# Kernel optimization log

Measured on AMD Instinct MI355X. Metric: run time of the kernel, lower is better.

## Reference

```python
import jax, jax.numpy as jnp
import numpy as np

B, N, DEG = 8, 8192, 16
E = B * N * DEG
K1 = 2458  # ceil(0.3*8192)
K2 = 738   # ceil(0.3*2458)
NUM_CLASSES = 10


def gat(x, src, dst, emask, W, a_s, a_d, bias):
    # PyG GATConv with add_self_loops=True, negative_slope=0.2, concat heads
    n = x.shape[0]
    H, F = a_s.shape
    xp = (x @ W).reshape(n, H, F)                      # [n,H,F]
    al_s = (xp * a_s).sum(-1)                          # [n,H]
    al_d = (xp * a_d).sum(-1)
    loops = jnp.arange(n, dtype=src.dtype)
    s2 = jnp.concatenate([src, loops])
    d2 = jnp.concatenate([dst, loops])
    m2 = jnp.concatenate([emask, jnp.ones(n, bool)])
    e = jax.nn.leaky_relu(al_s[s2] + al_d[d2], 0.2)    # [E+n,H]
    e = jnp.where(m2[:, None], e, -1e9)
    emax = jax.ops.segment_max(e, d2, num_segments=n)
    ex = jnp.where(m2[:, None], jnp.exp(e - emax[d2]), 0.0)
    den = jax.ops.segment_sum(ex, d2, num_segments=n)
    msg = ex[:, :, None] * xp[s2]                      # [E+n,H,F]
    out = jax.ops.segment_sum(msg, d2, num_segments=n) / den[:, :, None]
    return out.reshape(n, H * F) + bias


def inorm(x):
    # PyG InstanceNorm (affine=False): per-graph per-channel normalization
    xb = x.reshape(B, -1, x.shape[-1])
    mu = xb.mean(1, keepdims=True)
    var = ((xb - mu) ** 2).mean(1, keepdims=True)
    return ((xb - mu) / jnp.sqrt(var + 1e-5)).reshape(x.shape)


def topk_pool(x, src, dst, emask, p, k):
    # TopKPooling: score = tanh(x.p/|p|), keep top-k per graph, scale x by score
    n_tot = x.shape[0]
    n = n_tot // B
    score = jnp.tanh((x @ p) / jnp.linalg.norm(p))
    sv, si = jax.lax.top_k(score.reshape(B, n), k)     # [B,k]
    xg = jnp.take_along_axis(x.reshape(B, n, -1), si[:, :, None], axis=1)
    xnew = (xg * sv[:, :, None]).reshape(B * k, -1)
    perm = (si + (jnp.arange(B) * n)[:, None]).reshape(-1)
    newid = jnp.full(n_tot, -1, dtype=src.dtype).at[perm].set(
        jnp.arange(B * k, dtype=src.dtype))
    ns, nd = newid[src], newid[dst]
    m = emask & (ns >= 0) & (nd >= 0)
    return xnew, jnp.maximum(ns, 0), jnp.maximum(nd, 0), m


def setup_inputs() -> dict:
    key = jax.random.key(0)
    ks = jax.random.split(key, 32)
    pos = jax.random.normal(ks[0], (B * N, 3), jnp.float32)
    offs = jnp.repeat(jnp.arange(B, dtype=jnp.int32) * N, N * DEG)
    src = jax.random.randint(ks[1], (E,), 0, N, jnp.int32) + offs
    dst = jax.random.randint(ks[2], (E,), 0, N, jnp.int32) + offs

    def lin(k, fi, fo):
        return jax.random.normal(k, (fi, fo), jnp.float32) * (1.0 / np.sqrt(fi))

    d = dict(pos=pos, src=src, dst=dst)
    d['W1'] = lin(ks[3], 3, 32);   d['a_s1'] = jax.random.normal(ks[4], (2, 16)) * 0.2
    d['a_d1'] = jax.random.normal(ks[5], (2, 16)) * 0.2
    d['b1'] = jnp.zeros((32,));    d['p1'] = jax.random.normal(ks[6], (32,))
    d['W2'] = lin(ks[7], 32, 128); d['a_s2'] = jax.random.normal(ks[8], (2, 64)) * 0.2
    d['a_d2'] = jax.random.normal(ks[9], (2, 64)) * 0.2
    d['b2'] = jnp.zeros((128,));   d['p2'] = jax.random.normal(ks[10], (128,))
    d['W3'] = lin(ks[11], 128, 256); d['a_s3'] = jax.random.normal(ks[12], (1, 256)) * 0.1
    d['a_d3'] = jax.random.normal(ks[13], (1, 256)) * 0.1
    d['b3'] = jnp.zeros((256,))
    d['gw1'] = lin(ks[14], 256, 64);  d['gb1'] = jnp.zeros((64,))
    d['gw2'] = lin(ks[15], 64, 1);    d['gb2'] = jnp.zeros((1,))
    d['aw'] = lin(ks[16], 256, 256);  d['ab'] = jnp.zeros((256,))
    d['w1'] = lin(ks[17], 256, 512);  d['bb1'] = jnp.zeros((512,))
    d['w2'] = lin(ks[18], 512, 128);  d['bb2'] = jnp.zeros((128,))
    d['w3'] = lin(ks[19], 128, NUM_CLASSES); d['bb3'] = jnp.zeros((NUM_CLASSES,))
    return d


def reference(pos, src, dst, W1, a_s1, a_d1, b1, p1, W2, a_s2, a_d2, b2, p2,
              W3, a_s3, a_d3, b3, gw1, gb1, gw2, gb2, aw, ab,
              w1, bb1, w2, bb2, w3, bb3):
    emask = jnp.ones(src.shape[0], bool)
    x = gat(pos, src, dst, emask, W1, a_s1, a_d1, b1)
    x = jax.nn.elu(inorm(x))
    x, src, dst, emask = topk_pool(x, src, dst, emask, p1, K1)
    x = gat(x, src, dst, emask, W2, a_s2, a_d2, b2)
    x = jax.nn.elu(inorm(x))
    x, src, dst, emask = topk_pool(x, src, dst, emask, p2, K2)
    x = gat(x, src, dst, emask, W3, a_s3, a_d3, b3)
    x = jax.nn.elu(inorm(x))
    # GlobalAttention: gate_nn = Linear(256,64)+ELU+Linear(64,1); nn = Linear+ELU
    gate = jax.nn.elu(x @ gw1 + gb1) @ gw2 + gb2       # [M,1]
    h = jax.nn.elu(x @ aw + ab)                        # [M,256]
    a = jax.nn.softmax(gate.reshape(B, K2, 1), axis=1)
    g = (a * h.reshape(B, K2, 256)).sum(1)             # [B,256]
    z = jax.nn.elu(g @ w1 + bb1)   # dropout inactive in eval
    z = jax.nn.elu(z @ w2 + bb2)
    z = z @ w3 + bb3
    return jax.nn.log_softmax(z, axis=1)
```

## Files before the change

kernel.cpp:

```cpp
#include <hip/hip_runtime.h>
#include <cstdint>
#include <cstddef>

#define DI __device__ __forceinline__

namespace pk {

constexpr int NB1 = 65536;
constexpr int NE  = 1048576;
constexpr int BG  = 8;
constexpr int NPG1 = 8192;
constexpr int EPG1 = NE/BG;
constexpr int KP1 = 2458;
constexpr int KP2 = 738;
constexpr int NN2 = BG*KP1;
constexpr int NN3 = BG*KP2;
constexpr int REG2 = 16384;
constexpr int REG3 = 4096;
constexpr int CAP2 = BG*REG2;
constexpr int CAP3 = BG*REG3;
constexpr int CPB1 = 8;
constexpr int NTILE = 32;
constexpr int BKT = 5120;

DI float lrelu(float x){ return x > 0.f ? x : 0.2f*x; }
DI float eluf(float x){ return x > 0.f ? x : expf(x) - 1.f; }

DI int swz_block(){
  int nb = gridDim.x, b = blockIdx.x;
  if((nb & 7) == 0) return (b & 7)*(nb >> 3) + (b >> 3);
  return b;
}

__global__ __launch_bounds__(1024) void k_s1_front(
    const float* __restrict__ pos, const float* __restrict__ W,
    const float* __restrict__ as_, const float* __restrict__ ad_,
    float* __restrict__ xp, float* __restrict__ als, float* __restrict__ ald,
    const int* __restrict__ se, const int* __restrict__ de,
    int* __restrict__ part, int* __restrict__ bcur, int* __restrict__ bpk){
  __shared__ int h[NPG1];
  __shared__ int hbase[NTILE];
  __shared__ int hc[NTILE];
  int tid = threadIdx.x;
  if(blockIdx.x < 64){
    int i = blockIdx.x*1024 + tid;
    float p0=pos[3*i], p1=pos[3*i+1], p2=pos[3*i+2];
    float row[32];
#pragma unroll
    for(int c=0;c<32;c++) row[c] = p0*W[c] + p1*W[32+c] + p2*W[64+c];
    float s0=0.f,d0=0.f,s1=0.f,d1=0.f;
#pragma unroll
    for(int f=0;f<16;f++){
      s0 += row[f]*as_[f];        d0 += row[f]*ad_[f];
      s1 += row[16+f]*as_[16+f];  d1 += row[16+f]*ad_[16+f];
    }
    float4* o = reinterpret_cast<float4*>(xp + (size_t)i*32);
#pragma unroll
    for(int q=0;q<8;q++) o[q] = make_float4(row[4*q],row[4*q+1],row[4*q+2],row[4*q+3]);
    als[2*i]=s0; als[2*i+1]=s1; ald[2*i]=d0; ald[2*i+1]=d1;
    return;
  }
  int bb = blockIdx.x - 64;
  int g = bb & 7, t = bb >> 3;
  for(int i=tid;i<NPG1;i+=1024) h[i]=0;
  __syncthreads();
  const int4* de4 = (const int4*)(de + g*EPG1 + t*(EPG1/CPB1));
  const int4* se4 = (const int4*)(se + g*EPG1 + t*(EPG1/CPB1));
  int lo = g*NPG1;
  int4 dv[4], sv[4];
#pragma unroll
  for(int j=0;j<4;j++){ dv[j]=de4[j*1024+tid]; sv[j]=se4[j*1024+tid]; }
  int dl[16], sl[16];
#pragma unroll
  for(int j=0;j<4;j++){
    dl[4*j+0]=dv[j].x-lo; dl[4*j+1]=dv[j].y-lo; dl[4*j+2]=dv[j].z-lo; dl[4*j+3]=dv[j].w-lo;
    sl[4*j+0]=sv[j].x-lo; sl[4*j+1]=sv[j].y-lo; sl[4*j+2]=sv[j].z-lo; sl[4*j+3]=sv[j].w-lo;
  }
#pragma unroll
  for(int q=0;q<16;q++) atomicAdd(&h[dl[q]],1);
  __syncthreads();
  if(tid < NTILE){
    int ssum = 0;
    for(int i=0;i<256;i++) ssum += h[tid*256+i];
    hbase[tid] = atomicAdd(&bcur[g*NTILE+tid], ssum);
    hc[tid] = 0;
  }
  int* pp = part + (size_t)(g*CPB1+t)*NPG1;
  for(int i=tid;i<NPG1;i+=1024) pp[i]=h[i];
  __syncthreads();
#pragma unroll
  for(int q=0;q<16;q++){
    int tt = dl[q] >> 8;
    int p = atomicAdd(&hc[tt],1) + hbase[tt];
    bpk[(size_t)(g*NTILE+tt)*BKT + p] = (sl[q]<<13) | dl[q];
  }
}

__global__ __launch_bounds__(1024) void k_scan1(
    const int* __restrict__ part, int* __restrict__ cnt,
    int* __restrict__ rowptr){
  __shared__ int wsum[16];
  int g = blockIdx.x;
  int tid = threadIdx.x, lane = tid & 63, w = tid >> 6;
  constexpr int PER = NPG1/1024;
  int base = g*NPG1;
  int i0 = tid*PER;
  int v[PER]; int s = 0;
#pragma unroll
  for(int j=0;j<PER;j++){
    int i = i0+j;
    int x = 0;
#pragma unroll
    for(int p=0;p<CPB1;p++) x += part[(size_t)(g*CPB1+p)*NPG1 + i];
    cnt[base+i] = x;
    v[j] = s; s += x;
  }
  int inc = s;
  for(int o=1;o<64;o<<=1){ int t2=__shfl_up(inc,o,64); if(lane>=o) inc+=t2; }
  if(lane==63) wsum[w]=inc;
  __syncthreads();
  int wb=0;
  for(int k=0;k<w;k++) wb+=wsum[k];
  int tb = g*EPG1 + wb + inc - s;
#pragma unroll
  for(int j=0;j<PER;j++) rowptr[base+i0+j] = tb + v[j];
}

__global__ __launch_bounds__(1024) void k_scatter_b(
    const int* __restrict__ bcur, const int* __restrict__ bpk,
    const int* __restrict__ rowptr, int* __restrict__ eo){
  __shared__ int cur[256];
  int tid = threadIdx.x;
  int g = blockIdx.x & 7, t = blockIdx.x >> 3;
  int lo = g*NPG1 + t*256;
  if(tid < 256) cur[tid] = rowptr[lo + tid];
  __syncthreads();
  int cnt = bcur[g*NTILE + t];
  const int* bp = bpk + (size_t)(g*NTILE + t)*BKT;
  for(int i=tid; i<cnt; i+=1024){
    int pk = bp[i];
    int dlo = pk & 8191;
    int slo = pk >> 13;
    int p = atomicAdd(&cur[dlo - t*256], 1);
    eo[p] = g*NPG1 + slo;
  }
}

__global__ __launch_bounds__(256) void k_scatter_r(
    const int* __restrict__ se, const int* __restrict__ de,
    const int* __restrict__ gcnt, int reg,
    int* __restrict__ cursor, int* __restrict__ eo){
  int i = swz_block()*256 + threadIdx.x;
  int g = i / reg, loc = i % reg;
  if(loc < gcnt[g]){
    int p = atomicAdd(&cursor[de[i]], 1);
    eo[p] = se[i];
  }
}

__global__ __launch_bounds__(256) void k_edge_compact(
    const int* __restrict__ se, const int* __restrict__ de,
    const int* __restrict__ gcnt_in, int fixed_in, int bpg, int reg_in,
    const int* __restrict__ newid, int* __restrict__ gcnt_out,
    int* __restrict__ ons, int* __restrict__ ond, int reg_out,
    int* __restrict__ cnt){
  __shared__ int s_a[4096];
  __shared__ int s_b[4096];
  __shared__ int run, tbase;
  int tid = threadIdx.x;
  if(tid == 0) run = 0;
  __syncthreads();
  int blk = swz_block();
  int g = blk / bpg, t = blk % bpg;
  int mg = gcnt_in ? gcnt_in[g] : fixed_in;
  if(mg > reg_in) mg = reg_in;
  int base_l = t*4096;
  if(base_l < mg){
    const int* deb = de + (size_t)g*reg_in + base_l;
    const int* seb = se + (size_t)g*reg_in + base_l;
    const int4* de4 = (const int4*)deb;
    const int4* se4 = (const int4*)seb;
    int4 BD[4], BS[4];
#pragma unroll
    for(int j=0;j<4;j++){ BD[j]=de4[j*256+tid]; BS[j]=se4[j*256+tid]; }
    int cl = 0;
#pragma unroll
    for(int j=0;j<4;j++){
      int eb = base_l + (j*256+tid)*4;
      int dd[4]={BD[j].x,BD[j].y,BD[j].z,BD[j].w};
      int ss[4]={BS[j].x,BS[j].y,BS[j].z,BS[j].w};
#pragma unroll
      for(int q=0;q<4;q++){
        if(eb+q < mg){
          int a = newid[ss[q]], b = newid[dd[q]];
          if(a>=0 && b>=0){ cl++; atomicAdd(&cnt[b], 1); }
        }
      }
    }
    int p0 = 0;
    if(cl) p0 = atomicAdd(&run, cl);
#pragma unroll
    for(int j=0;j<4;j++){
      int eb = base_l + (j*256+tid)*4;
      int dd[4]={BD[j].x,BD[j].y,BD[j].z,BD[j].w};
      int ss[4]={BS[j].x,BS[j].y,BS[j].z,BS[j].w};
#pragma unroll
      for(int q=0;q<4;q++){
        if(eb+q < mg){
          int a = newid[ss[q]], b = newid[dd[q]];
          if(a>=0 && b>=0){ s_a[p0]=a; s_b[p0]=b; p0++; }
        }
      }
    }
  }
  __syncthreads();
  int ns = run;
  if(tid==0) tbase = ns ? atomicAdd(&gcnt_out[g], ns) : 0;
  __syncthreads();
  int tb = tbase;
  for(int j=tid; j<ns; j+=256){
    int s2 = tb + j;
    if(s2 < reg_out){ ons[(size_t)g*reg_out+s2]=s_a[j]; ond[(size_t)g*reg_out+s2]=s_b[j]; }
  }
}

template<int PER>
DI void scan256(const int* __restrict__ cnt, int R, int estride,
                int* __restrict__ rowptr, int* __restrict__ cursor, int g){
  __shared__ int wsum[4];
  int tid = threadIdx.x, lane = tid & 63, w = tid >> 6;
  int base = g*R;
  int i0 = tid*PER;
  int v[PER]; int s = 0;
#pragma unroll
  for(int j=0;j<PER;j++){ int i=i0+j; int x=(i<R)?cnt[base+i]:0; v[j]=s; s+=x; }
  int inc = s;
  for(int o=1;o<64;o<<=1){ int t=__shfl_up(inc,o,64); if(lane>=o) inc+=t; }
  if(lane==63) wsum[w]=inc;
  __syncthreads();
  int wb=0;
  for(int k=0;k<w;k++) wb+=wsum[k];
  int tb = g*estride + wb + inc - s;
#pragma unroll
  for(int j=0;j<PER;j++){
    int i=i0+j;
    if(i<R){
      int e=tb+v[j];
      rowptr[base+i]=e;
      cursor[base+i]=e;
    }
  }
}

template<int H,int F,int EB>
__global__ __launch_bounds__(256) void k_gat_fused(
    const float* __restrict__ xp, const float* __restrict__ als,
    const float* __restrict__ ald, const int* __restrict__ rowptr,
    const int* __restrict__ cnt, const int* __restrict__ esrc,
    const float* __restrict__ bias, float* __restrict__ out,
    float* __restrict__ accum, int RPG, int bpg){
  constexpr int C = H*F, C4 = C/4;
  constexpr int NPB = 256/C4;
  __shared__ float psum[4][C], psq[4][C];
  int tid = threadIdx.x;
  int nl = tid / C4, p = tid % C4;
  int work = (blockIdx.x & 7)*(gridDim.x >> 3) + (blockIdx.x >> 3);
  int g = work / bpg, t = work - g*bpg;
  int loc = t*NPB + nl;
  int node = g*RPG + loc;
  int hh = (4*p)/F;
  const float4* xp4 = (const float4*)xp;
  float4 r = make_float4(0.f,0.f,0.f,0.f);
  bool valid = loc < RPG;
  if(valid){
    float dvh = ald[node*H+hh];
    float sw  = expf(lrelu(als[node*H+hh] + dvh));
    float4 xs = xp4[(size_t)node*C4 + p];
    float den = sw;
    float ax=sw*xs.x, ay=sw*xs.y, az=sw*xs.z, aw_=sw*xs.w;
    int r0  = rowptr[node];
    int deg = cnt[node];
    for(int j=0; j<deg; j+=EB){
      int idx[EB]; float wv[EB]; float4 v[EB];
#pragma unroll
      for(int q=0;q<EB;q++)
        idx[q] = (j+q < deg) ? esrc[r0+j+q] : node;
#pragma unroll
      for(int q=0;q<EB;q++)
        wv[q] = als[idx[q]*H+hh];
#pragma unroll
      for(int q=0;q<EB;q++)
        v[q] = xp4[(size_t)idx[q]*C4 + p];
#pragma unroll
      for(int q=0;q<EB;q++){
        float w = (j+q < deg) ? expf(lrelu(wv[q] + dvh)) : 0.f;
        den += w;
        ax += w*v[q].x; ay += w*v[q].y; az += w*v[q].z; aw_ += w*v[q].w;
      }
    }
    float inv = 1.f / den;
    float4 bv = ((const float4*)bias)[p];
    r.x=ax*inv+bv.x; r.y=ay*inv+bv.y; r.z=az*inv+bv.z; r.w=aw_*inv+bv.w;
    ((float4*)out)[(size_t)node*C4 + p] = r;
  }
  float sx=r.x, sy=r.y, sz=r.z, sw2=r.w;
  float qx=r.x*r.x, qy=r.y*r.y, qz=r.z*r.z, qw=r.w*r.w;
#pragma unroll
  for(int off=C4; off<64; off<<=1){
    sx += __shfl_down(sx, off, 64); sy += __shfl_down(sy, off, 64);
    sz += __shfl_down(sz, off, 64); sw2 += __shfl_down(sw2, off, 64);
    qx += __shfl_down(qx, off, 64); qy += __shfl_down(qy, off, 64);
    qz += __shfl_down(qz, off, 64); qw += __shfl_down(qw, off, 64);
  }
  int lane = tid & 63, w = tid >> 6;
  if(lane < C4){
    psum[w][4*lane+0]=sx; psum[w][4*lane+1]=sy;
    psum[w][4*lane+2]=sz; psum[w][4*lane+3]=sw2;
    psq[w][4*lane+0]=qx;  psq[w][4*lane+1]=qy;
    psq[w][4*lane+2]=qz;  psq[w][4*lane+3]=qw;
  }
  __syncthreads();
  if(tid < C){
    float ts = psum[0][tid]+psum[1][tid]+psum[2][tid]+psum[3][tid];
    float tq = psq[0][tid]+psq[1][tid]+psq[2][tid]+psq[3][tid];
    atomicAdd(&accum[(g*C+tid)*2],   ts);
    atomicAdd(&accum[(g*C+tid)*2+1], tq);
  }
}

DI float inorm_of(const float* accum, int gc, float R, float x){
  float s = accum[gc*2], sq = accum[gc*2+1];
  float mu = s / R;
  float var = fmaxf(sq/R - mu*mu, 0.f);
  return eluf((x-mu)*rsqrtf(var+1e-5f));
}

template<int K,int CO,int NPG,int H,int PER>
__global__ __launch_bounds__(256) void k_gemm_al(
    const float* __restrict__ X, const float* __restrict__ naccum, int nRPG,
    const int* __restrict__ oldid,
    const float* __restrict__ scale, const float* __restrict__ W,
    float* __restrict__ Y, const float* __restrict__ a_s,
    const float* __restrict__ a_d, float* __restrict__ als,
    float* __restrict__ ald, int n, int ngemm,
    const int* __restrict__ scnt, int sR, int sstride,
    int* __restrict__ srowptr, int* __restrict__ scursor){
  constexpr int SUB = 256/CO;
  constexpr int NB = SUB*NPG;
  __shared__ float xs[NB][K];
  __shared__ float ps[4][NPG], pd[4][NPG];
  if((int)blockIdx.x >= ngemm){
    scan256<PER>(scnt, sR, sstride, srowptr, scursor, (int)blockIdx.x - ngemm);
    return;
  }
  int tid = threadIdx.x;
  int c = tid % CO, sg = tid / CO;
  int n0 = blockIdx.x * NB;
  for(int idx=tid; idx<NB*K; idx+=256){
    int r = idx / K, k = idx % K;
    int row = n0 + r;
    float v = 0.f;
    if(row < n){
      int orow = oldid[row];
      int og = orow / nRPG;
      v = inorm_of(naccum, og*K + k, (float)nRPG, X[(size_t)orow*K + k]) * scale[row];
    }
    xs[r][k] = v;
  }
  __syncthreads();
  float acc[NPG];
#pragma unroll
  for(int q=0;q<NPG;q++) acc[q]=0.f;
  for(int k=0;k<K;k++){
    float wv = W[(size_t)k*CO + c];
#pragma unroll
    for(int q=0;q<NPG;q++) acc[q] += xs[sg*NPG+q][k]*wv;
  }
  float asc = a_s[c], adc = a_d[c];
  float vs[NPG], vd[NPG];
#pragma unroll
  for(int q=0;q<NPG;q++){
    int row = n0 + sg*NPG + q;
    if(row < n) Y[(size_t)row*CO + c] = acc[q];
    vs[q] = acc[q]*asc; vd[q] = acc[q]*adc;
  }
#pragma unroll
  for(int o=32;o>0;o>>=1){
#pragma unroll
    for(int q=0;q<NPG;q++){
      vs[q] += __shfl_down(vs[q], o, 64);
      vd[q] += __shfl_down(vd[q], o, 64);
    }
  }
  int lane = tid & 63, w = tid >> 6;
  if(H == 2){
    if(lane == 0){
      int sg_ = w >> 1, h = w & 1;
#pragma unroll
      for(int q=0;q<NPG;q++){
        int row = n0 + sg_*NPG + q;
        if(row < n){ als[row*2+h] = vs[q]; ald[row*2+h] = vd[q]; }
      }
    }
  } else {
    if(lane == 0){
#pragma unroll
      for(int q=0;q<NPG;q++){ ps[w][q]=vs[q]; pd[w][q]=vd[q]; }
    }
    __syncthreads();
    if(tid < NPG){
      float s=0.f, d=0.f;
      for(int ww=0;ww<4;ww++){ s+=ps[ww][tid]; d+=pd[ww][tid]; }
      int row = n0 + tid;
      if(row < n){ als[row]=s; ald[row]=d; }
    }
  }
}

template<int C>
__global__ __launch_bounds__(256) void k_inorm_score(
    const float* __restrict__ x, const float* __restrict__ accum,
    const float* __restrict__ p, int R, int total,
    float* __restrict__ score, unsigned* __restrict__ u){
  __shared__ float rvp[256], rpp[256];
  int tid = threadIdx.x;
  int i = blockIdx.x*256 + tid;
  int c = tid & (C-1);
  bool act = i < total;
  float v = 0.f, pv = 0.f;
  if(act){
    int g = i / (R*C);
    v = inorm_of(accum, g*C+c, (float)R, x[i]);
    pv = p[c];
  }
  rvp[tid] = v*pv; rpp[tid] = pv*pv;
  __syncthreads();
#pragma unroll
  for(int s2=C/2; s2>0; s2>>=1){
    if(c < s2){ rvp[tid]+=rvp[tid+s2]; rpp[tid]+=rpp[tid+s2]; }
    __syncthreads();
  }
  if(act && c==0){
    float sv = tanhf(rvp[tid]*rsqrtf(rpp[tid]));
    int row = i / C;
    score[row] = sv;
    unsigned bts = __float_as_uint(sv);
    u[row] = (bts & 0x80000000u) ? ~bts : (bts | 0x80000000u);
  }
}

__global__ __launch_bounds__(1024) void k_topk(
    const unsigned* __restrict__ u, const float* __restrict__ score,
    int R, int Ksel, int* __restrict__ newid, int* __restrict__ oldid,
    float* __restrict__ scale){
  __shared__ int hist[2048];
  __shared__ int seg[32];
  __shared__ int sh_b, sh_k;
  __shared__ int wsA[16], wsB[16];
  __shared__ int carr0, carr1;
  int g = blockIdx.x, tid = threadIdx.x, lane = tid&63, w = tid>>6;
  const unsigned* ug = u + (size_t)g*R;
  unsigned prefix = 0;
  int K = Ksel;
  for(int lev=0; lev<3; lev++){
    int shf = (lev==0)?21:((lev==1)?10:0);
    int nb  = (lev==2)?1024:2048;
    for(int i=tid;i<2048;i+=1024) hist[i]=0;
    __syncthreads();
    for(int i=tid;i<R;i+=1024){
      unsigned v = ug[i];
      bool ok = (lev==0) || (lev==1 && (v>>21)==prefix) || (lev==2 && (v>>10)==prefix);
      if(ok) atomicAdd(&hist[(v>>shf)&(nb-1)], 1);
    }
    __syncthreads();
    int W = nb/32;
    if(tid<32){ int s=0; int lo=nb-W*(tid+1); for(int b=lo;b<lo+W;b++) s+=hist[b]; seg[tid]=s; }
    __syncthreads();
    if(tid==0){
      int kk=K, sgi=0;
      while(seg[sgi]<kk){ kk-=seg[sgi]; sgi++; }
      int b = nb-1-W*sgi;
      while(hist[b]<kk){ kk-=hist[b]; b--; }
      sh_b=b; sh_k=kk;
    }
    __syncthreads();
    int b = sh_b; K = sh_k;
    if(lev==0) prefix = (unsigned)b;
    else if(lev==1) prefix = (prefix<<11) | (unsigned)b;
    else prefix = (prefix<<10) | (unsigned)b;
    __syncthreads();
  }
  unsigned thr = prefix;
  int need = K;
  if(tid==0){ carr0=0; carr1=0; }
  __syncthreads();
  for(int bb=0; bb<R; bb+=1024){
    int i = bb + tid; bool in = i < R;
    unsigned uv = in ? ug[i] : 0u;
    int eq = (in && uv==thr) ? 1:0;
    int gt = (in && uv>thr) ? 1:0;
    int inc = eq;
    for(int o=1;o<64;o<<=1){ int t=__shfl_up(inc,o,64); if(lane>=o) inc+=t; }
    if(lane==63) wsA[w]=inc;
    __syncthreads();
    int wb=0; for(int k=0;k<w;k++) wb+=wsA[k];
    int eq_excl = carr0 + wb + inc - eq;
    int take = (gt || (eq && eq_excl<need)) ? 1 : 0;
    int inc2 = take;
    for(int o=1;o<64;o<<=1){ int t=__shfl_up(inc2,o,64); if(lane>=o) inc2+=t; }
    if(lane==63) wsB[w]=inc2;
    __syncthreads();
    int wb2=0; for(int k=0;k<w;k++) wb2+=wsB[k];
    int pos = carr1 + wb2 + inc2 - take;
    if(take){
      int nr = g*Ksel + pos;
      newid[(size_t)g*R+i] = nr;
      oldid[nr] = g*R+i;
      scale[nr] = score[(size_t)g*R+i];
    }
    __syncthreads();
    if(tid==1023){ carr0 += wb + inc; carr1 += wb2 + inc2; }
    __syncthreads();
  }
}

__global__ __launch_bounds__(256) void k_gate_fused(
    const float* __restrict__ X, const float* __restrict__ accum,
    const float* __restrict__ gw1, const float* __restrict__ gb1,
    const float* __restrict__ gw2, const float* __restrict__ gb2,
    float* __restrict__ gatev, int n){
  __shared__ float xs[8][256];
  int tid = threadIdx.x;
  int n0 = blockIdx.x*8;
  for(int idx=tid; idx<2048; idx+=256){
    int r = idx >> 8, k = idx & 255;
    int row = n0 + r;
    float v = 0.f;
    if(row < n){
      int g = row / KP2;
      v = inorm_of(accum, g*256+k, (float)KP2, X[(size_t)row*256 + k]);
    }
    xs[r][k] = v;
  }
  __syncthreads();
  int sg = tid >> 6, c = tid & 63;
  float a0 = 0.f, a1 = 0.f;
#pragma unroll 8
  for(int k=0;k<256;k++){
    float w = gw1[k*64+c];
    a0 = fmaf(xs[sg][k],   w, a0);
    a1 = fmaf(xs[sg+4][k], w, a1);
  }
  float gb = gb1[c], g2 = gw2[c];
  float v0 = eluf(a0 + gb) * g2;
  float v1 = eluf(a1 + gb) * g2;
#pragma unroll
  for(int o=32;o>0;o>>=1){
    v0 += __shfl_down(v0, o, 64);
    v1 += __shfl_down(v1, o, 64);
  }
  if(c==0){
    int r0 = n0 + sg, r1 = n0 + sg + 4;
    if(r0 < n) gatev[r0] = v0 + gb2[0];
    if(r1 < n) gatev[r1] = v1 + gb2[0];
  }
}

__global__ __launch_bounds__(256) void k_attn_gemm(
    const float* __restrict__ X, const float* __restrict__ accum,
    const float* __restrict__ W, const float* __restrict__ bias,
    const float* __restrict__ gatev, float* __restrict__ gvec){
  __shared__ float xs[8][256];
  __shared__ float red[256];
  int tid = threadIdx.x;
  int t = blockIdx.x, g = blockIdx.y;
  int r0 = t*8;
  float mx = -1e30f;
  for(int r=tid;r<KP2;r+=256) mx = fmaxf(mx, gatev[g*KP2+r]);
  red[tid]=mx; __syncthreads();
  for(int s=128;s>0;s>>=1){ if(tid<s) red[tid]=fmaxf(red[tid],red[tid+s]); __syncthreads(); }
  mx = red[0]; __syncthreads();
  float sm=0.f;
  for(int r=tid;r<KP2;r+=256) sm += expf(gatev[g*KP2+r]-mx);
  red[tid]=sm; __syncthreads();
  for(int s=128;s>0;s>>=1){ if(tid<s) red[tid]+=red[tid+s]; __syncthreads(); }
  float inv = 1.f/red[0];
  __syncthreads();
  for(int idx=tid; idx<2048; idx+=256){
    int r = idx >> 8, k = idx & 255;
    int lr = r0 + r;
    float v = 0.f;
    if(lr < KP2){
      int row = g*KP2 + lr;
      v = inorm_of(accum, g*256+k, (float)KP2, X[(size_t)row*256 + k]);
    }
    xs[r][k] = v;
  }
  __syncthreads();
  int c = tid;
  float acc[8];
#pragma unroll
  for(int q=0;q<8;q++) acc[q]=0.f;
  for(int k=0;k<256;k++){
    float wv = W[(size_t)k*256 + c];
#pragma unroll
    for(int q=0;q<8;q++) acc[q] += xs[q][k]*wv;
  }
  float bv = bias[c];
  float tot = 0.f;
#pragma unroll
  for(int q=0;q<8;q++){
    int lr = r0 + q;
    if(lr < KP2){
      float h = eluf(acc[q] + bv);
      tot += expf(gatev[g*KP2+lr]-mx) * h;
    }
  }
  atomicAdd(&gvec[g*256+c], tot*inv);
}

template<int K,int CO,int ACT>
__global__ __launch_bounds__(256) void k_mlp_t(
    const float* __restrict__ X, const float* __restrict__ W,
    const float* __restrict__ b, float* __restrict__ Y, int n){
  int i = blockIdx.x*256+threadIdx.x;
  if(i>=n*CO) return;
  int r=i/CO, c=i%CO;
  const float* xr = X + (size_t)r*K;
  float a=0.f;
#pragma unroll 16
  for(int k=0;k<K;k++) a = fmaf(xr[k], W[(size_t)k*CO+c], a);
  a += b[c];
  if(ACT) a = eluf(a);
  Y[i]=a;
}

__global__ __launch_bounds__(64) void k_head(
    const float* __restrict__ z2, const float* __restrict__ w3,
    const float* __restrict__ b3, float* __restrict__ out){
  __shared__ float zc[10]; __shared__ float mred, sred;
  int g=blockIdx.x, tid=threadIdx.x;
  if(tid<10){
    float a=0.f;
#pragma unroll 16
    for(int k=0;k<128;k++) a += z2[g*128+k]*w3[k*10+tid];
    zc[tid]=a+b3[tid];
  }
  __syncthreads();
  if(tid==0){
    float m=zc[0];
    for(int k=1;k<10;k++) m=fmaxf(m,zc[k]);
    float s=0.f;
    for(int k=0;k<10;k++) s+=expf(zc[k]-m);
    mred=m; sred=logf(s);
  }
  __syncthreads();
  if(tid<10) out[g*10+tid]=zc[tid]-mred-sred;
}

}

extern "C" void kernel_launch(void* const* d_in, const int* in_sizes, int n_in,
                              void* d_out, int out_size, void* d_ws, size_t ws_size,
                              hipStream_t stream){
  using namespace pk;
  (void)in_sizes; (void)n_in; (void)out_size;
  const float* pos = (const float*)d_in[0];
  const int*   src = (const int*)d_in[1];
  const int*   dst = (const int*)d_in[2];
  const float* W1  = (const float*)d_in[3];
  const float* as1 = (const float*)d_in[4];
  const float* ad1 = (const float*)d_in[5];
  const float* b1  = (const float*)d_in[6];
  const float* p1  = (const float*)d_in[7];
  const float* W2  = (const float*)d_in[8];
  const float* as2 = (const float*)d_in[9];
  const float* ad2 = (const float*)d_in[10];
  const float* b2  = (const float*)d_in[11];
  const float* p2  = (const float*)d_in[12];
  const float* W3  = (const float*)d_in[13];
  const float* as3 = (const float*)d_in[14];
  const float* ad3 = (const float*)d_in[15];
  const float* b3  = (const float*)d_in[16];
  const float* gw1 = (const float*)d_in[17];
  const float* gb1 = (const float*)d_in[18];
  const float* gw2 = (const float*)d_in[19];
  const float* gb2 = (const float*)d_in[20];
  const float* aw  = (const float*)d_in[21];
  const float* ab  = (const float*)d_in[22];
  const float* w1  = (const float*)d_in[23];
  const float* bb1 = (const float*)d_in[24];
  const float* w2  = (const float*)d_in[25];
  const float* bb2 = (const float*)d_in[26];
  const float* w3  = (const float*)d_in[27];
  const float* bb3 = (const float*)d_in[28];
  float* out = (float*)d_out;

  char* base = (char*)d_ws; size_t off = 0;
  auto alloc = [&](size_t nbytes)->char*{
    char* p = base + off; off = (off + nbytes + 255) & ~(size_t)255; return p;
  };
  int*   cnt2  = (int*)alloc((size_t)NN2*4);
  int*   cnt3  = (int*)alloc((size_t)NN3*4);
  int*   ecnt2 = (int*)alloc((size_t)BG*4);
  int*   ecnt3 = (int*)alloc((size_t)BG*4);
  float* acc1  = (float*)alloc((size_t)BG*32*2*4);
  float* acc2  = (float*)alloc((size_t)BG*128*2*4);
  float* acc3  = (float*)alloc((size_t)BG*256*2*4);
  float* gvec  = (float*)alloc((size_t)BG*256*4);
  int*   bcur1 = (int*)alloc((size_t)BG*NTILE*4);
  size_t zend = off;
  int*   newid1 = (int*)alloc((size_t)NB1*4);
  int*   newid2 = (int*)alloc((size_t)NN2*4);
  size_t fstart = (size_t)((char*)newid1 - base);
  size_t fend = off;
  int*      part1  = (int*)alloc((size_t)BG*CPB1*NPG1*4);
  int*      cnt1   = (int*)alloc((size_t)NB1*4);
  int*      bpk1   = (int*)alloc((size_t)BG*NTILE*BKT*4);
  float*    xp1    = (float*)alloc((size_t)NB1*32*4);
  float*    als1   = (float*)alloc((size_t)NB1*2*4);
  float*    ald1   = (float*)alloc((size_t)NB1*2*4);
  int*      rowptr1= (int*)alloc((size_t)NB1*4);
  int*      esrc1  = (int*)alloc((size_t)NE*4);
  float*    out1   = (float*)alloc((size_t)NB1*32*4);
  float*    score1 = (float*)alloc((size_t)NB1*4);
  unsigned* u1     = (unsigned*)alloc((size_t)NB1*4);
  int*      oldid1 = (int*)alloc((size_t)NN2*4);
  float*    scale1 = (float*)alloc((size_t)NN2*4);
  int*      ns2    = (int*)alloc((size_t)CAP2*4);
  int*      nd2    = (int*)alloc((size_t)CAP2*4);
  int*      rowptr2= (int*)alloc((size_t)NN2*4);
  int*      cursor2= (int*)alloc((size_t)NN2*4);
  int*      esrc2  = (int*)alloc((size_t)CAP2*4);
  float*    xp2    = (float*)alloc((size_t)NN2*128*4);
  float*    als2   = (float*)alloc((size_t)NN2*2*4);
  float*    ald2   = (float*)alloc((size_t)NN2*2*4);
  float*    out2   = (float*)alloc((size_t)NN2*128*4);
  float*    score2 = (float*)alloc((size_t)NN2*4);
  unsigned* u2     = (unsigned*)alloc((size_t)NN2*4);
  int*      oldid2 = (int*)alloc((size_t)NN3*4);
  float*    scale2 = (float*)alloc((size_t)NN3*4);
  int*      ns3    = (int*)alloc((size_t)CAP3*4);
  int*      nd3    = (int*)alloc((size_t)CAP3*4);
  int*      rowptr3= (int*)alloc((size_t)NN3*4);
  int*      cursor3= (int*)alloc((size_t)NN3*4);
  int*      esrc3  = (int*)alloc((size_t)CAP3*4);
  float*    xp3    = (float*)alloc((size_t)NN3*256*4);
  float*    als3   = (float*)alloc((size_t)NN3*4);
  float*    ald3   = (float*)alloc((size_t)NN3*4);
  float*    out3   = (float*)alloc((size_t)NN3*256*4);
  float*    gatev  = (float*)alloc((size_t)NN3*4);
  float*    z1     = (float*)alloc((size_t)BG*512*4);
  float*    z2     = (float*)alloc((size_t)BG*128*4);
  if(off > ws_size) return;

  auto cdiv = [](int a, int b){ return (a+b-1)/b; };

  hipMemsetAsync(base, 0, zend, stream);
  hipMemsetAsync(base + fstart, 0xFF, fend - fstart, stream);

  k_s1_front<<<128,1024,0,stream>>>(pos,W1,as1,ad1,xp1,als1,ald1,src,dst,part1,bcur1,bpk1);
  k_scan1<<<BG,1024,0,stream>>>(part1,cnt1,rowptr1);
  k_scatter_b<<<256,1024,0,stream>>>(bcur1,bpk1,rowptr1,esrc1);
  k_gat_fused<2,16,16><<<2048,256,0,stream>>>(xp1,als1,ald1,rowptr1,cnt1,esrc1,b1,out1,acc1,NPG1,256);
  k_inorm_score<32><<<cdiv(NB1*32,256),256,0,stream>>>(out1,acc1,p1,8192,NB1*32,score1,u1);
  k_topk<<<BG,1024,0,stream>>>(u1,score1,8192,KP1,newid1,oldid1,scale1);
  k_edge_compact<<<BG*32,256,0,stream>>>(src,dst,nullptr,EPG1,32,EPG1,newid1,ecnt2,ns2,nd2,REG2,cnt2);
  {
    int ngemm = cdiv(NN2,8);
    k_gemm_al<32,128,4,2,10><<<ngemm+BG,256,0,stream>>>(
        out1,acc1,NPG1,oldid1,scale1,W2,xp2,as2,ad2,als2,ald2,NN2,
        ngemm,cnt2,KP1,REG2,rowptr2,cursor2);
  }
  k_scatter_r<<<CAP2/256,256,0,stream>>>(ns2,nd2,ecnt2,REG2,cursor2,esrc2);
  k_gat_fused<2,64,8><<<8*308,256,0,stream>>>(xp2,als2,ald2,rowptr2,cnt2,esrc2,b2,out2,acc2,KP1,308);
  k_inorm_score<128><<<cdiv(NN2*128,256),256,0,stream>>>(out2,acc2,p2,KP1,NN2*128,score2,u2);
  k_topk<<<BG,1024,0,stream>>>(u2,score2,KP1,KP2,newid2,oldid2,scale2);
  k_edge_compact<<<BG*4,256,0,stream>>>(ns2,nd2,ecnt2,0,4,REG2,newid2,ecnt3,ns3,nd3,REG3,cnt3);
  {
    int ngemm = cdiv(NN3,4);
    k_gemm_al<128,256,4,1,3><<<ngemm+BG,256,0,stream>>>(
        out2,acc2,KP1,oldid2,scale2,W3,xp3,as3,ad3,als3,ald3,NN3,
        ngemm,cnt3,KP2,REG3,rowptr3,cursor3);
  }
  k_scatter_r<<<CAP3/256,256,0,stream>>>(ns3,nd3,ecnt3,REG3,cursor3,esrc3);
  k_gat_fused<1,256,4><<<8*185,256,0,stream>>>(xp3,als3,ald3,rowptr3,cnt3,esrc3,b3,out3,acc3,KP2,185);
  k_gate_fused<<<cdiv(NN3,8),256,0,stream>>>(out3,acc3,gw1,gb1,gw2,gb2,gatev,NN3);
  k_attn_gemm<<<dim3(cdiv(KP2,8),BG),256,0,stream>>>(out3,acc3,aw,ab,gatev,gvec);
  k_mlp_t<256,512,1><<<cdiv(BG*512,256),256,0,stream>>>(gvec,w1,bb1,z1,BG);
  k_mlp_t<512,128,1><<<cdiv(BG*128,256),256,0,stream>>>(z1,w2,bb2,z2,BG);
  k_head<<<BG,64,0,stream>>>(z2,w3,bb3,out);
}
```

Measured before the change: 408.6 us.

## Fuse edge compaction into GEMM launch, split scan out, double stage-1 edge blocks

```diff
diff --git a/kernel.cpp b/kernel.cpp
--- a/kernel.cpp
+++ b/kernel.cpp
@@ -19,7 +19,7 @@
 constexpr int REG3 = 4096;
 constexpr int CAP2 = BG*REG2;
 constexpr int CAP3 = BG*REG3;
-constexpr int CPB1 = 8;
+constexpr int CPB1 = 16;
 constexpr int NTILE = 32;
 constexpr int BKT = 5120;
 
@@ -67,17 +67,17 @@
   const int4* de4 = (const int4*)(de + g*EPG1 + t*(EPG1/CPB1));
   const int4* se4 = (const int4*)(se + g*EPG1 + t*(EPG1/CPB1));
   int lo = g*NPG1;
-  int4 dv[4], sv[4];
-#pragma unroll
-  for(int j=0;j<4;j++){ dv[j]=de4[j*1024+tid]; sv[j]=se4[j*1024+tid]; }
-  int dl[16], sl[16];
-#pragma unroll
-  for(int j=0;j<4;j++){
+  int4 dv[2], sv[2];
+#pragma unroll
+  for(int j=0;j<2;j++){ dv[j]=de4[j*1024+tid]; sv[j]=se4[j*1024+tid]; }
+  int dl[8], sl[8];
+#pragma unroll
+  for(int j=0;j<2;j++){
     dl[4*j+0]=dv[j].x-lo; dl[4*j+1]=dv[j].y-lo; dl[4*j+2]=dv[j].z-lo; dl[4*j+3]=dv[j].w-lo;
     sl[4*j+0]=sv[j].x-lo; sl[4*j+1]=sv[j].y-lo; sl[4*j+2]=sv[j].z-lo; sl[4*j+3]=sv[j].w-lo;
   }
 #pragma unroll
-  for(int q=0;q<16;q++) atomicAdd(&h[dl[q]],1);
+  for(int q=0;q<8;q++) atomicAdd(&h[dl[q]],1);
   __syncthreads();
   if(tid < NTILE){
     int ssum = 0;
@@ -89,7 +89,7 @@
   for(int i=tid;i<NPG1;i+=1024) pp[i]=h[i];
   __syncthreads();
 #pragma unroll
-  for(int q=0;q<16;q++){
+  for(int q=0;q<8;q++){
     int tt = dl[q] >> 8;
     int p = atomicAdd(&hc[tt],1) + hbase[tt];
     bpk[(size_t)(g*NTILE+tt)*BKT + p] = (sl[q]<<13) | dl[q];
@@ -158,72 +158,6 @@
   }
 }
 
-__global__ __launch_bounds__(256) void k_edge_compact(
-    const int* __restrict__ se, const int* __restrict__ de,
-    const int* __restrict__ gcnt_in, int fixed_in, int bpg, int reg_in,
-    const int* __restrict__ newid, int* __restrict__ gcnt_out,
-    int* __restrict__ ons, int* __restrict__ ond, int reg_out,
-    int* __restrict__ cnt){
-  __shared__ int s_a[4096];
-  __shared__ int s_b[4096];
-  __shared__ int run, tbase;
-  int tid = threadIdx.x;
-  if(tid == 0) run = 0;
-  __syncthreads();
-  int blk = swz_block();
-  int g = blk / bpg, t = blk % bpg;
-  int mg = gcnt_in ? gcnt_in[g] : fixed_in;
-  if(mg > reg_in) mg = reg_in;
-  int base_l = t*4096;
-  if(base_l < mg){
-    const int* deb = de + (size_t)g*reg_in + base_l;
-    const int* seb = se + (size_t)g*reg_in + base_l;
-    const int4* de4 = (const int4*)deb;
-    const int4* se4 = (const int4*)seb;
-    int4 BD[4], BS[4];
-#pragma unroll
-    for(int j=0;j<4;j++){ BD[j]=de4[j*256+tid]; BS[j]=se4[j*256+tid]; }
-    int cl = 0;
-#pragma unroll
-    for(int j=0;j<4;j++){
-      int eb = base_l + (j*256+tid)*4;
-      int dd[4]={BD[j].x,BD[j].y,BD[j].z,BD[j].w};
-      int ss[4]={BS[j].x,BS[j].y,BS[j].z,BS[j].w};
-#pragma unroll
-      for(int q=0;q<4;q++){
-        if(eb+q < mg){
-          int a = newid[ss[q]], b = newid[dd[q]];
-          if(a>=0 && b>=0){ cl++; atomicAdd(&cnt[b], 1); }
-        }
-      }
-    }
-    int p0 = 0;
-    if(cl) p0 = atomicAdd(&run, cl);
-#pragma unroll
-    for(int j=0;j<4;j++){
-      int eb = base_l + (j*256+tid)*4;
-      int dd[4]={BD[j].x,BD[j].y,BD[j].z,BD[j].w};
-      int ss[4]={BS[j].x,BS[j].y,BS[j].z,BS[j].w};
-#pragma unroll
-      for(int q=0;q<4;q++){
-        if(eb+q < mg){
-          int a = newid[ss[q]], b = newid[dd[q]];
-          if(a>=0 && b>=0){ s_a[p0]=a; s_b[p0]=b; p0++; }
-        }
-      }
-    }
-  }
-  __syncthreads();
-  int ns = run;
-  if(tid==0) tbase = ns ? atomicAdd(&gcnt_out[g], ns) : 0;
-  __syncthreads();
-  int tb = tbase;
-  for(int j=tid; j<ns; j+=256){
-    int s2 = tb + j;
-    if(s2 < reg_out){ ons[(size_t)g*reg_out+s2]=s_a[j]; ond[(size_t)g*reg_out+s2]=s_b[j]; }
-  }
-}
-
 template<int PER>
 DI void scan256(const int* __restrict__ cnt, int R, int estride,
                 int* __restrict__ rowptr, int* __restrict__ cursor, int g){
@@ -250,6 +184,20 @@
       cursor[base+i]=e;
     }
   }
+}
+
+template<int PER>
+__global__ __launch_bounds__(256) void k_scan_w(
+    const int* __restrict__ cnt, int R, int estride,
+    int* __restrict__ rowptr, int* __restrict__ cursor){
+  scan256<PER>(cnt, R, estride, rowptr, cursor, (int)blockIdx.x);
+}
+
+DI float inorm_of(const float* accum, int gc, float R, float x){
+  float s = accum[gc*2], sq = accum[gc*2+1];
+  float mu = s / R;
+  float var = fmaxf(sq/R - mu*mu, 0.f);
+  return eluf((x-mu)*rsqrtf(var+1e-5f));
 }
 
 template<int H,int F,int EB>
@@ -328,34 +276,86 @@
   }
 }
 
-DI float inorm_of(const float* accum, int gc, float R, float x){
-  float s = accum[gc*2], sq = accum[gc*2+1];
-  float mu = s / R;
-  float var = fmaxf(sq/R - mu*mu, 0.f);
-  return eluf((x-mu)*rsqrtf(var+1e-5f));
-}
-
-template<int K,int CO,int NPG,int H,int PER>
-__global__ __launch_bounds__(256) void k_gemm_al(
+template<int K,int CO,int NPG,int H,int CHUNK>
+__global__ __launch_bounds__(256) void k_cpt_gemm(
+    const int* __restrict__ se, const int* __restrict__ de,
+    const int* __restrict__ gcnt_in, int fixed_in, int reg_in,
+    const int* __restrict__ newid, int* __restrict__ gcnt_out,
+    int* __restrict__ ons, int* __restrict__ ond, int reg_out,
+    int* __restrict__ cnt, int ncomp,
     const float* __restrict__ X, const float* __restrict__ naccum, int nRPG,
-    const int* __restrict__ oldid,
-    const float* __restrict__ scale, const float* __restrict__ W,
-    float* __restrict__ Y, const float* __restrict__ a_s,
-    const float* __restrict__ a_d, float* __restrict__ als,
-    float* __restrict__ ald, int n, int ngemm,
-    const int* __restrict__ scnt, int sR, int sstride,
-    int* __restrict__ srowptr, int* __restrict__ scursor){
+    const int* __restrict__ oldid, const float* __restrict__ scale,
+    const float* __restrict__ W, float* __restrict__ Y,
+    const float* __restrict__ a_s, const float* __restrict__ a_d,
+    float* __restrict__ als, float* __restrict__ ald, int n){
   constexpr int SUB = 256/CO;
   constexpr int NB = SUB*NPG;
-  __shared__ float xs[NB][K];
+  static_assert(NB*K <= 2*CHUNK, "xs must fit the union");
+  __shared__ int sm[2*CHUNK];
+  __shared__ int run, tbase;
   __shared__ float ps[4][NPG], pd[4][NPG];
-  if((int)blockIdx.x >= ngemm){
-    scan256<PER>(scnt, sR, sstride, srowptr, scursor, (int)blockIdx.x - ngemm);
+  int tid = threadIdx.x;
+  if((int)blockIdx.x < ncomp){
+    int* s_a = sm;
+    int* s_b = sm + CHUNK;
+    if(tid == 0) run = 0;
+    __syncthreads();
+    int blk = blockIdx.x;
+    int g = blk & 7, t = blk >> 3;
+    int mg = gcnt_in ? gcnt_in[g] : fixed_in;
+    if(mg > reg_in) mg = reg_in;
+    int base_l = t*CHUNK;
+    if(base_l < mg){
+      const int4* de4 = (const int4*)(de + (size_t)g*reg_in + base_l);
+      const int4* se4 = (const int4*)(se + (size_t)g*reg_in + base_l);
+      int4 BD[CHUNK/1024], BS[CHUNK/1024];
+#pragma unroll
+      for(int j=0;j<CHUNK/1024;j++){ BD[j]=de4[j*256+tid]; BS[j]=se4[j*256+tid]; }
+      int cl = 0;
+#pragma unroll
+      for(int j=0;j<CHUNK/1024;j++){
+        int eb = base_l + (j*256+tid)*4;
+        int dd[4]={BD[j].x,BD[j].y,BD[j].z,BD[j].w};
+        int ss[4]={BS[j].x,BS[j].y,BS[j].z,BS[j].w};
+#pragma unroll
+        for(int q=0;q<4;q++){
+          if(eb+q < mg){
+            int a = newid[ss[q]], b = newid[dd[q]];
+            if(a>=0 && b>=0){ cl++; atomicAdd(&cnt[b], 1); }
+          }
+        }
+      }
+      int p0 = 0;
+      if(cl) p0 = atomicAdd(&run, cl);
+#pragma unroll
+      for(int j=0;j<CHUNK/1024;j++){
+        int eb = base_l + (j*256+tid)*4;
+        int dd[4]={BD[j].x,BD[j].y,BD[j].z,BD[j].w};
+        int ss[4]={BS[j].x,BS[j].y,BS[j].z,BS[j].w};
+#pragma unroll
+        for(int q=0;q<4;q++){
+          if(eb+q < mg){
+            int a = newid[ss[q]], b = newid[dd[q]];
+            if(a>=0 && b>=0){ s_a[p0]=a; s_b[p0]=b; p0++; }
+          }
+        }
+      }
+    }
+    __syncthreads();
+    int ns = run;
+    if(tid==0) tbase = ns ? atomicAdd(&gcnt_out[blockIdx.x & 7], ns) : 0;
+    __syncthreads();
+    int tb = tbase;
+    int g2 = blockIdx.x & 7;
+    for(int j=tid; j<ns; j+=256){
+      int s2 = tb + j;
+      if(s2 < reg_out){ ons[(size_t)g2*reg_out+s2]=s_a[j]; ond[(size_t)g2*reg_out+s2]=s_b[j]; }
+    }
     return;
   }
-  int tid = threadIdx.x;
+  float (*xs)[K] = reinterpret_cast<float(*)[K]>(sm);
   int c = tid % CO, sg = tid / CO;
-  int n0 = blockIdx.x * NB;
+  int n0 = ((int)blockIdx.x - ncomp) * NB;
   for(int idx=tid; idx<NB*K; idx+=256){
     int r = idx / K, k = idx % K;
     int row = n0 + r;
@@ -759,30 +759,24 @@
   hipMemsetAsync(base, 0, zend, stream);
   hipMemsetAsync(base + fstart, 0xFF, fend - fstart, stream);
 
-  k_s1_front<<<128,1024,0,stream>>>(pos,W1,as1,ad1,xp1,als1,ald1,src,dst,part1,bcur1,bpk1);
+  k_s1_front<<<192,1024,0,stream>>>(pos,W1,as1,ad1,xp1,als1,ald1,src,dst,part1,bcur1,bpk1);
   k_scan1<<<BG,1024,0,stream>>>(part1,cnt1,rowptr1);
   k_scatter_b<<<256,1024,0,stream>>>(bcur1,bpk1,rowptr1,esrc1);
   k_gat_fused<2,16,16><<<2048,256,0,stream>>>(xp1,als1,ald1,rowptr1,cnt1,esrc1,b1,out1,acc1,NPG1,256);
   k_inorm_score<32><<<cdiv(NB1*32,256),256,0,stream>>>(out1,acc1,p1,8192,NB1*32,score1,u1);
   k_topk<<<BG,1024,0,stream>>>(u1,score1,8192,KP1,newid1,oldid1,scale1);
-  k_edge_compact<<<BG*32,256,0,stream>>>(src,dst,nullptr,EPG1,32,EPG1,newid1,ecnt2,ns2,nd2,REG2,cnt2);
-  {
-    int ngemm = cdiv(NN2,8);
-    k_gemm_al<32,128,4,2,10><<<ngemm+BG,256,0,stream>>>(
-        out1,acc1,NPG1,oldid1,scale1,W2,xp2,as2,ad2,als2,ald2,NN2,
-        ngemm,cnt2,KP1,REG2,rowptr2,cursor2);
-  }
+  k_cpt_gemm<32,128,4,2,2048><<<512+cdiv(NN2,8),256,0,stream>>>(
+      src,dst,nullptr,EPG1,EPG1,newid1,ecnt2,ns2,nd2,REG2,cnt2,512,
+      out1,acc1,NPG1,oldid1,scale1,W2,xp2,as2,ad2,als2,ald2,NN2);
+  k_scan_w<10><<<BG,256,0,stream>>>(cnt2,KP1,REG2,rowptr2,cursor2);
   k_scatter_r<<<CAP2/256,256,0,stream>>>(ns2,nd2,ecnt2,REG2,cursor2,esrc2);
   k_gat_fused<2,64,8><<<8*308,256,0,stream>>>(xp2,als2,ald2,rowptr2,cnt2,esrc2,b2,out2,acc2,KP1,308);
   k_inorm_score<128><<<cdiv(NN2*128,256),256,0,stream>>>(out2,acc2,p2,KP1,NN2*128,score2,u2);
   k_topk<<<BG,1024,0,stream>>>(u2,score2,KP1,KP2,newid2,oldid2,scale2);
-  k_edge_compact<<<BG*4,256,0,stream>>>(ns2,nd2,ecnt2,0,4,REG2,newid2,ecnt3,ns3,nd3,REG3,cnt3);
-  {
-    int ngemm = cdiv(NN3,4);
-    k_gemm_al<128,256,4,1,3><<<ngemm+BG,256,0,stream>>>(
-        out2,acc2,KP1,oldid2,scale2,W3,xp3,as3,ad3,als3,ald3,NN3,
-        ngemm,cnt3,KP2,REG3,rowptr3,cursor3);
-  }
+  k_cpt_gemm<128,256,4,1,2048><<<64+cdiv(NN3,4),256,0,stream>>>(
+      ns2,nd2,ecnt2,0,REG2,newid2,ecnt3,ns3,nd3,REG3,cnt3,64,
+      out2,acc2,KP1,oldid2,scale2,W3,xp3,as3,ad3,als3,ald3,NN3);
+  k_scan_w<3><<<BG,256,0,stream>>>(cnt3,KP2,REG3,rowptr3,cursor3);
   k_scatter_r<<<CAP3/256,256,0,stream>>>(ns3,nd3,ecnt3,REG3,cursor3,esrc3);
   k_gat_fused<1,256,4><<<8*185,256,0,stream>>>(xp3,als3,ald3,rowptr3,cnt3,esrc3,b3,out3,acc3,KP2,185);
   k_gate_fused<<<cdiv(NN3,8),256,0,stream>>>(out3,acc3,gw1,gb1,gw2,gb2,gatev,NN3);
```

New measurement: 395.3 us. -3.3%, faster.
